# Performance work log

Hardware: AMD Instinct MI355X
Metric: run time of the kernel (lower is better)

The kernel has to match this reference:

```python
import jax, jax.numpy as jnp
import numpy as np

# EctConfig constants
RESOLUTION = 64   # number of threshold steps
RADIUS = 1.1      # thresholds span [-RADIUS, RADIUS]
NUM_BATCHES = 64  # number of point clouds


def setup_inputs() -> dict:
    key = jax.random.key(0)
    k1, k2, k3 = jax.random.split(key, 3)
    N, D, T = 1048576, 3, 64
    x = jax.random.normal(k1, (N, D), dtype=jnp.float32) * 0.5  # points roughly inside radius
    v = jax.random.normal(k2, (D, T), dtype=jnp.float32)
    v = v / jnp.linalg.norm(v, axis=0, keepdims=True)  # unit directions [D, T]
    batch = jnp.sort(jax.random.randint(k3, (N,), 0, NUM_BATCHES)).astype(jnp.int64)
    return {"x": x, "v": v, "batch": batch, "num_batches": NUM_BATCHES}


def reference(x, v, batch, num_batches):
    # Projection of every point onto every direction: [N, T]
    nh = x @ v
    R = RESOLUTION
    T = v.shape[1]
    # Map each projected height to a threshold bin in [0, R-1]
    bins = jnp.clip(
        jnp.floor((nh + RADIUS) / (2.0 * RADIUS) * R), 0, R - 1
    ).astype(jnp.int32)  # [N, T]
    # Fused (batch, bin) index so a single scatter-add builds all histograms
    flat = batch[:, None].astype(jnp.int32) * R + bins  # [N, T]
    counts = jnp.zeros((num_batches * R, T), dtype=jnp.float32)
    counts = counts.at[flat, jnp.arange(T)[None, :]].add(1.0)
    # Cumulative count over thresholds = Euler characteristic curve per direction
    ect = jnp.cumsum(counts.reshape(num_batches, R, T), axis=1)  # [B, R, T]
    return ect
```

## Files before the change

### kernel.cpp

```cpp
#include <hip/hip_runtime.h>

#define RES 64
#define TD 64
#define NB 64
#define BLK 1024
#define WAVES 16
#define CHUNK 2048

__global__ __launch_bounds__(256) void ect_init_kernel(
    const int* __restrict__ batch, int N,
    float4* __restrict__ out4, int* __restrict__ offs)
{
    int gid = blockIdx.x * 256 + threadIdx.x;
    out4[gid] = float4{0.f, 0.f, 0.f, 0.f};
    if (blockIdx.x == 0 && threadIdx.x <= NB) {
        int val = (int)threadIdx.x;
        int lo = 0, hi = N;
        while (lo < hi) {
            int mid = (lo + hi) >> 1;
            if (batch[mid] < val) lo = mid + 1; else hi = mid;
        }
        offs[threadIdx.x] = lo;
    }
}

__global__ __launch_bounds__(BLK) void ect_hist_kernel(
    const float* __restrict__ x, const float* __restrict__ v,
    const int* __restrict__ offs, float* __restrict__ out, int N)
{
    const int start = blockIdx.x * CHUNK;
    const int stop  = min(start + CHUNK, N);
    if (start >= N) return;

    __shared__ unsigned hist[2][RES * TD];
    __shared__ unsigned col_part[TD][17];

    const int t = threadIdx.x & 63;
    const int w = threadIdx.x >> 6;
    unsigned* __restrict__ hwt = &hist[w >> 3][t];
    const float S = 64.0f / 2.2f;
    const float v0S = v[t] * S;
    const float v1S = v[TD + t] * S;
    const float v2S = v[2 * TD + t] * S;

    int lo = 0, hi = NB;
    while (lo < hi) {
        int mid = (lo + hi + 1) >> 1;
        if (offs[mid] <= start) lo = mid; else hi = mid - 1;
    }
    int b = lo;

#define SELREG(q, r0, r1, r2) ((q) < 64 ? (r0) : ((q) < 128 ? (r1) : (r2)))
#define RD(q, r0, r1, r2) __uint_as_float(__builtin_amdgcn_readlane(           \
        __float_as_uint(SELREG(q, r0, r1, r2)), (q) & 63))
#define PROC1(j, r0, r1, r2) {                                                 \
        float x0 = RD(3*(j), r0,r1,r2), x1 = RD(3*(j)+1, r0,r1,r2),            \
              x2 = RD(3*(j)+2, r0,r1,r2);                                      \
        float f = fmaf(x0, v0S, fmaf(x1, v1S, fmaf(x2, v2S, 32.0f)));          \
        f = __builtin_amdgcn_fmed3f(f, 0.0f, 63.0f);                           \
        int bin = (int)f;                                                      \
        atomicAdd(hwt + (bin << 6), 1u); }

    int seg = start;
    while (seg < stop) {
        while (offs[b + 1] <= seg) ++b;
        const int segend = min(stop, offs[b + 1]);

        for (int i = threadIdx.x; i < 2 * RES * TD; i += BLK) hist[0][i] = 0u;
        __syncthreads();

        const int npts = segend - seg;
        const int nf = npts >> 6;

        float c0, c1, c2, n0, n1, n2;
        int tl = w;
        if (tl < nf) {
            const int fb = 3 * (seg + (tl << 6)) + t;
            c0 = x[fb]; c1 = x[fb + 64]; c2 = x[fb + 128];
        }
        for (; tl < nf; tl += WAVES) {
            const int tn = tl + WAVES;
            if (tn < nf) {
                const int fb = 3 * (seg + (tn << 6)) + t;
                n0 = x[fb]; n1 = x[fb + 64]; n2 = x[fb + 128];
            }
            #pragma unroll
            for (int j = 0; j < 64; ++j) PROC1(j, c0, c1, c2);
            if (tn < nf) { c0 = n0; c1 = n1; c2 = n2; }
        }

        const int rem = npts & 63;
        if (rem && w == (nf & (WAVES - 1))) {
            const int fb = 3 * (seg + (nf << 6)) + t;
            const int lim = 3 * segend;
            float l0 = (fb       < lim) ? x[fb]       : 0.0f;
            float l1 = (fb +  64 < lim) ? x[fb +  64] : 0.0f;
            float l2 = (fb + 128 < lim) ? x[fb + 128] : 0.0f;
            #pragma unroll
            for (int j = 0; j < 64; ++j) {
                if (j < rem) PROC1(j, l0, l1, l2);
            }
        }
        __syncthreads();

        unsigned vals[4];
        {
            unsigned s = 0;
            #pragma unroll
            for (int i = 0; i < 4; ++i) {
                int r = (w << 2) + i;
                s += hist[0][(r << 6) + t] + hist[1][(r << 6) + t];
                vals[i] = s;
            }
            col_part[t][w] = s;
        }
        __syncthreads();
        {
            unsigned off = 0;
            for (int j = 0; j < w; ++j) off += col_part[t][j];
            float* __restrict__ gb = out + b * (RES * TD) + t;
            #pragma unroll
            for (int i = 0; i < 4; ++i) {
                int r = (w << 2) + i;
                atomicAdd(gb + (r << 6), (float)(vals[i] + off));
            }
        }
        if (segend < stop) __syncthreads();
        seg = segend;
    }
#undef PROC1
#undef RD
#undef SELREG
}

extern "C" void kernel_launch(void* const* d_in, const int* in_sizes, int n_in,
                              void* d_out, int out_size, void* d_ws, size_t ws_size,
                              hipStream_t stream) {
    const float* x = (const float*)d_in[0];
    const float* v = (const float*)d_in[1];
    const int* batch = (const int*)d_in[2];
    const int N = in_sizes[2];
    int* offs = (int*)d_ws;

    ect_init_kernel<<<(NB * RES * TD) / (256 * 4), 256, 0, stream>>>(
        batch, N, (float4*)d_out, offs);

    const int nblocks = (N + CHUNK - 1) / CHUNK;
    ect_hist_kernel<<<nblocks, BLK, 0, stream>>>(x, v, offs, (float*)d_out, N);
}
```

Before: 32.74 us.

## Find batch segments per block in shared memory and drop init kernel

The separate init kernel, which zeroed the output and binary-searched global batch offsets, is removed and its zeroing replaced with hipMemsetAsync. Each histogram block now loads its chunk of batch ids into LDS and builds a bitmask of segment boundaries, then finds segment ends with ffs. This is meant to cut a dependent kernel launch and the global offset lookups, at the cost of extra LDS use (about 8KB more), a chunk-wide batch read, and extra barriers in every block.

```diff
diff --git a/kernel.cpp b/kernel.cpp
--- a/kernel.cpp
+++ b/kernel.cpp
@@ -7,33 +7,19 @@
 #define WAVES 16
 #define CHUNK 2048
 
-__global__ __launch_bounds__(256) void ect_init_kernel(
-    const int* __restrict__ batch, int N,
-    float4* __restrict__ out4, int* __restrict__ offs)
-{
-    int gid = blockIdx.x * 256 + threadIdx.x;
-    out4[gid] = float4{0.f, 0.f, 0.f, 0.f};
-    if (blockIdx.x == 0 && threadIdx.x <= NB) {
-        int val = (int)threadIdx.x;
-        int lo = 0, hi = N;
-        while (lo < hi) {
-            int mid = (lo + hi) >> 1;
-            if (batch[mid] < val) lo = mid + 1; else hi = mid;
-        }
-        offs[threadIdx.x] = lo;
-    }
-}
-
 __global__ __launch_bounds__(BLK) void ect_hist_kernel(
     const float* __restrict__ x, const float* __restrict__ v,
-    const int* __restrict__ offs, float* __restrict__ out, int N)
+    const int* __restrict__ batch, float* __restrict__ out, int N)
 {
     const int start = blockIdx.x * CHUNK;
     const int stop  = min(start + CHUNK, N);
     if (start >= N) return;
+    const int len = stop - start;
 
     __shared__ unsigned hist[2][RES * TD];
     __shared__ unsigned col_part[TD][17];
+    __shared__ int      bchunk[CHUNK];
+    __shared__ unsigned bmask[CHUNK / 32];
 
     const int t = threadIdx.x & 63;
     const int w = threadIdx.x >> 6;
@@ -43,12 +29,14 @@
     const float v1S = v[TD + t] * S;
     const float v2S = v[2 * TD + t] * S;
 
-    int lo = 0, hi = NB;
-    while (lo < hi) {
-        int mid = (lo + hi + 1) >> 1;
-        if (offs[mid] <= start) lo = mid; else hi = mid - 1;
+    if (threadIdx.x < CHUNK / 32) bmask[threadIdx.x] = 0u;
+    for (int i = threadIdx.x; i < len; i += BLK) bchunk[i] = batch[start + i];
+    __syncthreads();
+    for (int i = threadIdx.x; i < len; i += BLK) {
+        bool bd = (i == len - 1) || (bchunk[i] != bchunk[i + 1]);
+        if (bd) atomicOr(&bmask[i >> 5], 1u << (i & 31));
     }
-    int b = lo;
+    __syncthreads();
 
 #define SELREG(q, r0, r1, r2) ((q) < 64 ? (r0) : ((q) < 128 ? (r1) : (r2)))
 #define RD(q, r0, r1, r2) __uint_as_float(__builtin_amdgcn_readlane(           \
@@ -63,8 +51,12 @@
 
     int seg = start;
     while (seg < stop) {
-        while (offs[b + 1] <= seg) ++b;
-        const int segend = min(stop, offs[b + 1]);
+        int word = (seg - start) >> 5;
+        unsigned m = bmask[word] & (0xFFFFFFFFu << ((seg - start) & 31));
+        while (m == 0u) m = bmask[++word];
+        const int bpos = (word << 5) + (__ffs(m) - 1);
+        const int segend = start + bpos + 1;
+        const int b = bchunk[bpos];
 
         for (int i = threadIdx.x; i < 2 * RES * TD; i += BLK) hist[0][i] = 0u;
         __syncthreads();
@@ -140,11 +132,9 @@
     const float* v = (const float*)d_in[1];
     const int* batch = (const int*)d_in[2];
     const int N = in_sizes[2];
-    int* offs = (int*)d_ws;
 
-    ect_init_kernel<<<(NB * RES * TD) / (256 * 4), 256, 0, stream>>>(
-        batch, N, (float4*)d_out, offs);
+    hipMemsetAsync(d_out, 0, (size_t)out_size * sizeof(float), stream);
 
     const int nblocks = (N + CHUNK - 1) / CHUNK;
-    ect_hist_kernel<<<nblocks, BLK, 0, stream>>>(x, v, offs, (float*)d_out, N);
+    ect_hist_kernel<<<nblocks, BLK, 0, stream>>>(x, v, batch, (float*)d_out, N);
 }
```

Result: slower. 35.95 us (+9.8%).
